# Kernel tuning notes

Hardware: AMD Instinct MI355X
Metric: run time of the kernel (lower is better)

## Reference

```python
import jax, jax.numpy as jnp
import numpy as np

H, W = 512, 512
G = 8192
ALPHA_THRESH = 1.0 / 255.0        # meta_f32[0]
TRANS_THRESH = 1.0e-4             # meta_f32[1]
ALPHA_CAP = 0.99                  # meta_f32[6]
BG = jnp.zeros((3,), dtype=jnp.float32)  # config.background


def setup_inputs() -> dict:
    key = jax.random.key(0)
    ks = jax.random.split(key, 7)
    mx = jax.random.uniform(ks[0], (G,), minval=0.0, maxval=float(W))
    my = jax.random.uniform(ks[1], (G,), minval=0.0, maxval=float(H))
    means2d = jnp.stack([mx, my], axis=-1)
    # Build valid conics (inverse 2x2 covariances) from random rotation + scales
    theta = jax.random.uniform(ks[2], (G,), minval=0.0, maxval=2.0 * np.pi)
    s = jax.random.uniform(ks[3], (G, 2), minval=2.0, maxval=12.0)  # px stddevs
    ct, st = jnp.cos(theta), jnp.sin(theta)
    v1, v2 = s[:, 0] ** 2, s[:, 1] ** 2
    ca = ct * ct * v1 + st * st * v2
    cb = ct * st * (v1 - v2)
    cc = st * st * v1 + ct * ct * v2
    det = ca * cc - cb * cb
    conics = jnp.stack([cc / det, -cb / det, ca / det], axis=-1)  # [G,3] = (a,b,c)
    colors = jax.random.uniform(ks[4], (G, 3))
    opacities = jax.random.uniform(ks[5], (G,))
    depths = jax.random.uniform(ks[6], (G,), minval=0.1, maxval=100.0)
    return {"means2d": means2d, "conics": conics, "colors": colors,
            "opacities": opacities, "depths": depths}


def reference(means2d, conics, colors, opacities, depths):
    # Stable front-to-back depth sort (mirrors perm = argsort(depths, stable))
    perm = jnp.argsort(depths, stable=True)
    m = means2d[perm]
    cn = conics[perm]
    col = colors[perm]
    op = opacities[perm]
    a, b, c = cn[:, 0], cn[:, 1], cn[:, 2]
    px = jnp.arange(W, dtype=means2d.dtype) + 0.5  # pixel centers

    def row(y):
        py = y.astype(means2d.dtype) + 0.5
        dx = px[:, None] - m[None, :, 0]          # [W,G]
        dy = py - m[:, 1]                          # [G]
        sigma = 0.5 * (a * dx * dx + c * dy * dy) + b * dx * dy  # [W,G]
        alpha = jnp.minimum(ALPHA_CAP, op * jnp.exp(-sigma))
        alpha = jnp.where((sigma < 0) | (alpha < ALPHA_THRESH), 0.0, alpha)
        # exclusive cumulative transmittance along depth order
        Tprev = jnp.cumprod(1.0 - alpha, axis=-1)
        Tprev = jnp.concatenate([jnp.ones((W, 1), alpha.dtype), Tprev[:, :-1]], axis=-1)
        # early-termination: splats seen after T drops below threshold contribute 0
        wgt = alpha * Tprev * (Tprev >= TRANS_THRESH)  # [W,G]
        rgb = wgt @ col                                 # [W,3]
        t_rem = 1.0 - wgt.sum(axis=-1)                  # remaining transmittance
        return rgb + t_rem[:, None] * BG

    return jax.lax.map(row, jnp.arange(H))  # [H,W,3]
```

## Files before the change

### kernel.cpp

```cpp
#include <hip/hip_runtime.h>

#define G 8192
#define IMG_W 512
#define IMG_H 512
#define TILE 16
#define NTX (IMG_W / TILE)
#define NTY (IMG_H / TILE)
#define BLK 256
#define CAP 1024
#define ALPHA_THRESH (1.0f/255.0f)
#define ALPHA_CAP 0.99f
#define TRANS_THRESH 1e-4f

__global__ __launch_bounds__(BLK)
void range_kernel(const float* __restrict__ means2d,
                  const float* __restrict__ conics,
                  const float* __restrict__ opac,
                  unsigned int* __restrict__ ranges)
{
    int g = blockIdx.x * BLK + threadIdx.x;
    if (g >= G) return;
    float op = opac[g];
    unsigned int packed = 0xFFu;
    if (op * 255.0f >= 1.0f) {
        float smax = __logf(op * 255.0f);
        float a = conics[3*g], b = conics[3*g+1], c = conics[3*g+2];
        float det = fmaxf(a * c - b * b, 1e-12f);
        float rx = sqrtf(fmaxf(2.0f * smax * c / det, 0.0f)) * 1.0001f + 0.01f;
        float ry = sqrtf(fmaxf(2.0f * smax * a / det, 0.0f)) * 1.0001f + 0.01f;
        float mx = means2d[2*g], my = means2d[2*g+1];
        int txmin = (int)ceilf ((mx - rx - 15.5f) * 0.0625f);
        int txmax = (int)floorf((mx + rx -  0.5f) * 0.0625f);
        int tymin = (int)ceilf ((my - ry - 15.5f) * 0.0625f);
        int tymax = (int)floorf((my + ry -  0.5f) * 0.0625f);
        if (!(txmax < 0 || txmin > NTX-1 || tymax < 0 || tymin > NTY-1 ||
              txmin > txmax || tymin > tymax)) {
            txmin = max(txmin, 0); txmax = min(txmax, NTX-1);
            tymin = max(tymin, 0); tymax = min(tymax, NTY-1);
            packed = (unsigned)txmin | ((unsigned)txmax << 8)
                   | ((unsigned)tymin << 16) | ((unsigned)tymax << 24);
        }
    }
    ranges[g] = packed;
}

__device__ __forceinline__ int hitp(unsigned p, unsigned btx, unsigned bty)
{
    return (btx >= (p & 0xffu)) & (btx <= ((p >> 8) & 0xffu)) &
           (bty >= ((p >> 16) & 0xffu)) & (bty <= (p >> 24));
}

__global__ __launch_bounds__(BLK)
void tile_kernel(const unsigned int* __restrict__ ranges,
                 const float* __restrict__ depths,
                 const float* __restrict__ means2d,
                 const float* __restrict__ conics,
                 const float* __restrict__ colors,
                 const float* __restrict__ opac,
                 float*       __restrict__ out)
{
    __shared__ unsigned short slist[CAP];
    __shared__ unsigned long long keys[CAP];
    __shared__ int woff[4];
    __shared__ float4 sq0[BLK];
    __shared__ float4 sq1[BLK];
    __shared__ float  sq2[BLK];

    const int tx = threadIdx.x, ty = threadIdx.y;
    const int t = ty * TILE + tx;
    const int lane = t & 63, w = t >> 6;
    const unsigned btx = blockIdx.x, bty = blockIdx.y;

    const uint4* r4 = (const uint4*)ranges;
    const int wbase = w * (G / 4);
    uint4 rv[8];
    #pragma unroll
    for (int i = 0; i < 8; ++i)
        rv[i] = r4[(wbase >> 2) + i * 64 + lane];

    int cnt = 0;
    #pragma unroll
    for (int i = 0; i < 8; ++i)
        cnt += hitp(rv[i].x, btx, bty) + hitp(rv[i].y, btx, bty)
             + hitp(rv[i].z, btx, bty) + hitp(rv[i].w, btx, bty);
    #pragma unroll
    for (int d = 1; d < 64; d <<= 1) cnt += __shfl_xor(cnt, d);
    if (lane == 0) woff[w] = cnt;
    __syncthreads();

    int offs = 0;
    for (int ww = 0; ww < w; ++ww) offs += woff[ww];
    const int N = min(woff[0] + woff[1] + woff[2] + woff[3], CAP);

    const unsigned long long lt = (1ull << lane) - 1ull;
    #pragma unroll
    for (int i = 0; i < 8; ++i) {
        int gbase = wbase + i * 256 + lane * 4;
        int h0 = hitp(rv[i].x, btx, bty), h1 = hitp(rv[i].y, btx, bty);
        int h2 = hitp(rv[i].z, btx, bty), h3 = hitp(rv[i].w, btx, bty);
        unsigned long long m0 = __ballot(h0), m1 = __ballot(h1);
        unsigned long long m2 = __ballot(h2), m3 = __ballot(h3);
        int pos = offs + __popcll(m0 & lt) + __popcll(m1 & lt)
                       + __popcll(m2 & lt) + __popcll(m3 & lt);
        if (h0) { if (pos < CAP) slist[pos] = (unsigned short)(gbase    ); pos++; }
        if (h1) { if (pos < CAP) slist[pos] = (unsigned short)(gbase + 1); pos++; }
        if (h2) { if (pos < CAP) slist[pos] = (unsigned short)(gbase + 2); pos++; }
        if (h3) { if (pos < CAP) slist[pos] = (unsigned short)(gbase + 3); pos++; }
        offs += __popcll(m0) + __popcll(m1) + __popcll(m2) + __popcll(m3);
    }
    __syncthreads();

    for (int i = t; i < N; i += BLK) {
        unsigned idx = slist[i];
        keys[i] = ((unsigned long long)__float_as_uint(depths[idx]) << 13)
                | (unsigned long long)idx;
    }
    __syncthreads();
    for (int i = t; i < N; i += BLK) {
        unsigned long long ke = keys[i];
        int r = 0;
        #pragma unroll 4
        for (int j = 0; j < N; ++j) r += (keys[j] < ke);
        slist[r] = (unsigned short)(ke & 0x1fffull);
    }
    __syncthreads();

    const float px = (float)(blockIdx.x * TILE + tx) + 0.5f;
    const float py = (float)(blockIdx.y * TILE + ty) + 0.5f;
    float T = 1.0f, accr = 0.0f, accg = 0.0f, accb = 0.0f;
    bool done = false;

    for (int base = 0; base < N; base += BLK) {
        int n = min(BLK, N - base);
        float4 v0 = make_float4(0.f, 0.f, 0.f, 0.f);
        float4 v1 = make_float4(0.f, 0.f, 0.f, 0.f);
        float  v2 = 0.f;
        if (t < n) {
            int idx = slist[base + t];
            v0 = make_float4(means2d[2*idx], means2d[2*idx+1],
                             conics[3*idx], conics[3*idx+1]);
            v1 = make_float4(conics[3*idx+2], opac[idx],
                             colors[3*idx], colors[3*idx+1]);
            v2 = colors[3*idx+2];
        }
        sq0[t] = v0; sq1[t] = v1; sq2[t] = v2;
        __syncthreads();

        if (!done) {
            int n4 = (n + 3) & ~3;
            for (int i = 0; i < n4 && !done; i += 4) {
                #pragma unroll
                for (int u = 0; u < 4; ++u) {
                    float4 q0 = sq0[i + u];
                    float4 q1 = sq1[i + u];
                    float  bl = sq2[i + u];
                    float dx = px - q0.x;
                    float dy = py - q0.y;
                    float sigma = 0.5f * (q0.z*dx*dx + q1.x*dy*dy)
                                + q0.w*dx*dy;
                    float al = q1.y * __expf(-sigma);
                    bool ok = (sigma >= 0.0f) && (al >= ALPHA_THRESH);
                    al = ok ? fminf(al, ALPHA_CAP) : 0.0f;
                    float wgt = al * T;
                    accr = fmaf(wgt, q1.z, accr);
                    accg = fmaf(wgt, q1.w, accg);
                    accb = fmaf(wgt, bl,   accb);
                    T *= (1.0f - al);
                }
                if (T < TRANS_THRESH) done = true;
            }
        }
        if (__syncthreads_and((int)done)) break;
    }

    const int o = ((blockIdx.y * TILE + ty) * IMG_W + blockIdx.x * TILE + tx) * 3;
    out[o]     = accr;
    out[o + 1] = accg;
    out[o + 2] = accb;
}

extern "C" void kernel_launch(void* const* d_in, const int* in_sizes, int n_in,
                              void* d_out, int out_size, void* d_ws, size_t ws_size,
                              hipStream_t stream)
{
    const float* means2d = (const float*)d_in[0];
    const float* conics  = (const float*)d_in[1];
    const float* colors  = (const float*)d_in[2];
    const float* opac    = (const float*)d_in[3];
    const float* depths  = (const float*)d_in[4];
    float* out = (float*)d_out;
    unsigned int* ranges = (unsigned int*)d_ws;

    range_kernel<<<G / BLK, BLK, 0, stream>>>(means2d, conics, opac, ranges);
    tile_kernel<<<dim3(NTX, NTY), dim3(TILE, TILE), 0, stream>>>(
        ranges, depths, means2d, conics, colors, opac, out);
}
```

Before: 88.97 us.

## Broadcast splat params via readlane per wave and shrink sort keys

Each wave now loads 64 sorted splats into registers and broadcasts them with readlane, replacing the block-wide shared-memory staging and its per-chunk __syncthreads. Early termination becomes per-wave via __all, so waves that finish early stop without waiting for the whole block. The depth sort uses 32-bit keys with an index tiebreak instead of 64-bit packed keys, which halves LDS traffic in the O(N^2) rank loop. In exchange each wave issues its own redundant global loads for the same splats, and readlane broadcasts are scalar-unit ops that may serialize.

```diff
diff --git a/kernel.cpp b/kernel.cpp
--- a/kernel.cpp
+++ b/kernel.cpp
@@ -50,6 +50,12 @@
            (bty >= ((p >> 16) & 0xffu)) & (bty <= (p >> 24));
 }
 
+__device__ __forceinline__ float rl(float v, int l)
+{
+    return __uint_as_float(__builtin_amdgcn_readlane(__float_as_uint(v),
+                                                     (unsigned)l));
+}
+
 __global__ __launch_bounds__(BLK)
 void tile_kernel(const unsigned int* __restrict__ ranges,
                  const float* __restrict__ depths,
@@ -60,11 +66,8 @@
                  float*       __restrict__ out)
 {
     __shared__ unsigned short slist[CAP];
-    __shared__ unsigned long long keys[CAP];
+    __shared__ unsigned int   fkeys[CAP];
     __shared__ int woff[4];
-    __shared__ float4 sq0[BLK];
-    __shared__ float4 sq1[BLK];
-    __shared__ float  sq2[BLK];
 
     const int tx = threadIdx.x, ty = threadIdx.y;
     const int t = ty * TILE + tx;
@@ -110,70 +113,79 @@
     }
     __syncthreads();
 
-    for (int i = t; i < N; i += BLK) {
-        unsigned idx = slist[i];
-        keys[i] = ((unsigned long long)__float_as_uint(depths[idx]) << 13)
-                | (unsigned long long)idx;
-    }
-    __syncthreads();
-    for (int i = t; i < N; i += BLK) {
-        unsigned long long ke = keys[i];
-        int r = 0;
-        #pragma unroll 4
-        for (int j = 0; j < N; ++j) r += (keys[j] < ke);
-        slist[r] = (unsigned short)(ke & 0x1fffull);
-    }
-    __syncthreads();
-
-    const float px = (float)(blockIdx.x * TILE + tx) + 0.5f;
-    const float py = (float)(blockIdx.y * TILE + ty) + 0.5f;
+    unsigned short myidx[4]; unsigned int mykey[4]; int myr[4];
+    #pragma unroll
+    for (int m = 0; m < 4; ++m) {
+        int i = t + m * BLK;
+        if (i < N) {
+            unsigned idx = slist[i];
+            unsigned k = __float_as_uint(depths[idx]);
+            myidx[m] = (unsigned short)idx; mykey[m] = k; fkeys[i] = k;
+        }
+    }
+    __syncthreads();
+    #pragma unroll
+    for (int m = 0; m < 4; ++m) {
+        int i = t + m * BLK;
+        if (i < N) {
+            unsigned ke = mykey[m]; int r = 0;
+            #pragma unroll 4
+            for (int j = 0; j < N; ++j) {
+                unsigned kj = fkeys[j];
+                r += (int)((kj < ke) | ((kj == ke) & (j < i)));
+            }
+            myr[m] = r;
+        }
+    }
+    __syncthreads();
+    #pragma unroll
+    for (int m = 0; m < 4; ++m) {
+        int i = t + m * BLK;
+        if (i < N) slist[myr[m]] = myidx[m];
+    }
+    __syncthreads();
+
+    const float px = (float)(btx * TILE + tx) + 0.5f;
+    const float py = (float)(bty * TILE + ty) + 0.5f;
     float T = 1.0f, accr = 0.0f, accg = 0.0f, accb = 0.0f;
-    bool done = false;
-
-    for (int base = 0; base < N; base += BLK) {
-        int n = min(BLK, N - base);
-        float4 v0 = make_float4(0.f, 0.f, 0.f, 0.f);
-        float4 v1 = make_float4(0.f, 0.f, 0.f, 0.f);
-        float  v2 = 0.f;
-        if (t < n) {
-            int idx = slist[base + t];
-            v0 = make_float4(means2d[2*idx], means2d[2*idx+1],
-                             conics[3*idx], conics[3*idx+1]);
-            v1 = make_float4(conics[3*idx+2], opac[idx],
-                             colors[3*idx], colors[3*idx+1]);
-            v2 = colors[3*idx+2];
-        }
-        sq0[t] = v0; sq1[t] = v1; sq2[t] = v2;
-        __syncthreads();
-
-        if (!done) {
-            int n4 = (n + 3) & ~3;
-            for (int i = 0; i < n4 && !done; i += 4) {
-                #pragma unroll
-                for (int u = 0; u < 4; ++u) {
-                    float4 q0 = sq0[i + u];
-                    float4 q1 = sq1[i + u];
-                    float  bl = sq2[i + u];
-                    float dx = px - q0.x;
-                    float dy = py - q0.y;
-                    float sigma = 0.5f * (q0.z*dx*dx + q1.x*dy*dy)
-                                + q0.w*dx*dy;
-                    float al = q1.y * __expf(-sigma);
-                    bool ok = (sigma >= 0.0f) && (al >= ALPHA_THRESH);
-                    al = ok ? fminf(al, ALPHA_CAP) : 0.0f;
-                    float wgt = al * T;
-                    accr = fmaf(wgt, q1.z, accr);
-                    accg = fmaf(wgt, q1.w, accg);
-                    accb = fmaf(wgt, bl,   accb);
-                    T *= (1.0f - al);
-                }
-                if (T < TRANS_THRESH) done = true;
+
+    for (int base = 0; base < N; base += 64) {
+        int nn = min(64, N - base);
+        int ll = (lane < nn) ? lane : 0;
+        int idx = slist[base + ll];
+        float mx = means2d[2*idx], my = means2d[2*idx+1];
+        float ha = conics[3*idx]   * 0.5f;
+        float hb = conics[3*idx+1];
+        float hc = conics[3*idx+2] * 0.5f;
+        float op = (lane < nn) ? opac[idx] : 0.0f;
+        float cr = colors[3*idx], cg = colors[3*idx+1], cbl = colors[3*idx+2];
+
+        int nn4 = (nn + 3) & ~3;
+        bool fin = false;
+        for (int j = 0; j < nn4; j += 4) {
+            #pragma unroll
+            for (int u = 0; u < 4; ++u) {
+                int l = j + u;
+                float smx = rl(mx, l), smy = rl(my, l);
+                float sa  = rl(ha, l), sb  = rl(hb, l), sc = rl(hc, l);
+                float sop = rl(op, l);
+                float dx = px - smx, dy = py - smy;
+                float sig = fmaf(sa, dx*dx, fmaf(sc, dy*dy, sb * (dx*dy)));
+                float al = sop * __expf(-sig);
+                bool ok = (sig >= 0.0f) && (al >= ALPHA_THRESH);
+                al = ok ? fminf(al, ALPHA_CAP) : 0.0f;
+                float wgt = al * T;
+                accr = fmaf(wgt, rl(cr, l),  accr);
+                accg = fmaf(wgt, rl(cg, l),  accg);
+                accb = fmaf(wgt, rl(cbl, l), accb);
+                T *= (1.0f - al);
             }
-        }
-        if (__syncthreads_and((int)done)) break;
-    }
-
-    const int o = ((blockIdx.y * TILE + ty) * IMG_W + blockIdx.x * TILE + tx) * 3;
+            if (__all(T < TRANS_THRESH)) { fin = true; break; }
+        }
+        if (fin) break;
+    }
+
+    const int o = (((int)bty * TILE + ty) * IMG_W + (int)btx * TILE + tx) * 3;
     out[o]     = accr;
     out[o + 1] = accg;
     out[o + 2] = accb;
```

Result: slower. 103.5 us (+16.3%).
